# Kernel optimization log

Hardware: AMD Instinct MI355X
Metric: run time of the kernel (lower is better)

## Reference

```python
import jax, jax.numpy as jnp
import numpy as np

T, B, S, H, E, V = 100, 64, 602, 1024, 512, 10000


def setup_inputs() -> dict:
    key = jax.random.key(0)
    ks = jax.random.split(key, 12)
    s = 0.02  # small init scale for numerical stability through tanh/sigmoid
    return {
        "tgt": jax.random.randint(ks[0], (T, B, 1), 0, V),
        "memory_bank": jax.random.normal(ks[1], (S, B, H), jnp.float32),
        "h0": jax.random.normal(ks[2], (2, B, H), jnp.float32) * 0.1,
        "c0": jax.random.normal(ks[3], (2, B, H), jnp.float32) * 0.1,
        "embedding": jax.random.normal(ks[4], (V, E), jnp.float32) * s,
        "Wi0": jax.random.normal(ks[5], (4 * H, E + H), jnp.float32) * s,
        "Wh0": jax.random.normal(ks[6], (4 * H, H), jnp.float32) * s,
        "bi0": jnp.zeros((4 * H,), jnp.float32),
        "bh0": jnp.zeros((4 * H,), jnp.float32),
        "Wi1": jax.random.normal(ks[7], (4 * H, H), jnp.float32) * s,
        "Wh1": jax.random.normal(ks[8], (4 * H, H), jnp.float32) * s,
        "bi1": jnp.zeros((4 * H,), jnp.float32),
        "bh1": jnp.zeros((4 * H,), jnp.float32),
        "W_attn": jax.random.normal(ks[9], (H, H), jnp.float32) * s,
        "W_out": jax.random.normal(ks[10], (H, 2 * H), jnp.float32) * s,
    }


def _lstm_cell(x, h, c, Wi, Wh, bi, bh):
    # PyTorch LSTM gate order: i, f, g, o
    g = x @ Wi.T + h @ Wh.T + bi + bh
    i, f, gg, o = jnp.split(g, 4, axis=-1)
    c2 = jax.nn.sigmoid(f) * c + jax.nn.sigmoid(i) * jnp.tanh(gg)
    h2 = jax.nn.sigmoid(o) * jnp.tanh(c2)
    return h2, c2


def reference(tgt, memory_bank, h0, c0, embedding, Wi0, Wh0, bi0, bh0,
              Wi1, Wh1, bi1, bh1, W_attn, W_out):
    emb = embedding[tgt[:, :, 0]]            # [T, B, E]
    M = jnp.transpose(memory_bank, (1, 0, 2))  # [B, S, H]

    def step(carry, e_t):
        hl0, hl1, cl0, cl1, feed = carry
        x = jnp.concatenate([e_t, feed], axis=-1)        # input feeding
        nh0, nc0 = _lstm_cell(x, hl0, cl0, Wi0, Wh0, bi0, bh0)
        nh1, nc1 = _lstm_cell(nh0, hl1, cl1, Wi1, Wh1, bi1, bh1)
        # GlobalAttention 'general': score = (h W) . m
        q = nh1 @ W_attn.T                                # [B, H]
        align = jnp.einsum('bh,bsh->bs', q, M)            # [B, S]
        a = jax.nn.softmax(align, axis=-1)
        ctx = jnp.einsum('bs,bsh->bh', a, M)              # [B, H]
        out = jnp.tanh(jnp.concatenate([ctx, nh1], -1) @ W_out.T)  # attn_h
        return (nh0, nh1, nc0, nc1, out), (out, a)

    init = (h0[0], h0[1], c0[0], c0[1], jnp.zeros((B, H), emb.dtype))
    (_, _, _, _, _), (outs, attns) = jax.lax.scan(step, init, emb)
    return outs, attns  # [T,B,H], [T,B,S]
```

## Files before the change

kernel.cpp:

```cpp
#include <hip/hip_runtime.h>


#define DI __device__ __forceinline__

typedef __attribute__((ext_vector_type(4))) short s4v;
typedef __attribute__((ext_vector_type(8))) short s8v;
typedef __attribute__((ext_vector_type(4))) float f4v;

DI float b2f(short u) {
  unsigned int x = ((unsigned int)(unsigned short)u) << 16;
  float f; __builtin_memcpy(&f, &x, 4); return f;
}
DI short f2b(float f) {
  unsigned int x; __builtin_memcpy(&x, &f, 4);
  return (short)((x + 0x7fffu + ((x >> 16) & 1u)) >> 16);
}
DI s8v cat8(s4v lo, s4v hi) {
  s8v r; r[0]=lo[0];r[1]=lo[1];r[2]=lo[2];r[3]=lo[3];
  r[4]=hi[0];r[5]=hi[1];r[6]=hi[2];r[7]=hi[3]; return r;
}
DI f4v mfma16(s8v a, s8v b, f4v c) {
  return __builtin_amdgcn_mfma_f32_16x16x32_bf16(a, b, c, 0, 0, 0);
}
DI float sigm(float x) { return 1.f / (1.f + __expf(-x)); }

DI unsigned long long ld64c(const void* p) {
  return __hip_atomic_load((const unsigned long long*)p, __ATOMIC_RELAXED,
                           __HIP_MEMORY_SCOPE_SYSTEM);
}
DI void st64c(void* p, unsigned long long v) {
  __hip_atomic_store((unsigned long long*)p, v, __ATOMIC_RELAXED,
                     __HIP_MEMORY_SCOPE_SYSTEM);
}
DI float ldfc(const float* p) {
  return __hip_atomic_load(p, __ATOMIC_RELAXED, __HIP_MEMORY_SCOPE_SYSTEM);
}
DI void stfc(float* p, float v) {
  __hip_atomic_store(p, v, __ATOMIC_RELAXED, __HIP_MEMORY_SCOPE_SYSTEM);
}
DI void st16c(short* p, short v) {
  asm volatile("global_store_short %0, %1, off sc0 sc1"
               :: "v"(p), "v"((unsigned int)(unsigned short)v) : "memory");
}
union U64S { unsigned long long u; short s[4]; };
union U64F { unsigned long long u; float f[2]; };


__global__ void cvt_bf16(const float* __restrict__ src, short* __restrict__ dst, long n8) {
  long i = (long)blockIdx.x * blockDim.x + threadIdx.x;
  long stride = (long)gridDim.x * blockDim.x;
  for (; i < n8; i += stride) {
    const float* s = src + i * 8;
    s8v o;
    #pragma unroll
    for (int j = 0; j < 8; ++j) o[j] = f2b(s[j]);
    *(s8v*)(dst + i * 8) = o;
  }
}

__global__ void pack_w(const float* __restrict__ WA, int Ka,
                       const float* __restrict__ WB, int Kb,
                       short* __restrict__ dst, int N, long total) {
  long i = (long)blockIdx.x * blockDim.x + threadIdx.x;
  long stride = (long)gridDim.x * blockDim.x;
  for (; i < total; i += stride) {
    int c = (int)(i & 3);
    long r = i >> 2;
    int n = (int)(r % N);
    int kt = (int)(r / N);
    int k = kt * 32 + c * 8;
    const float* s = (k < Ka) ? (WA + (size_t)n * Ka + k)
                              : (WB + (size_t)n * Kb + (k - Ka));
    s8v o;
    #pragma unroll
    for (int j = 0; j < 8; ++j) o[j] = f2b(s[j]);
    *(s8v*)(dst + r * 32 + c * 8) = o;
  }
}

__global__ __launch_bounds__(64) void emb_gather(const int* __restrict__ tgt,
                                                 const float* __restrict__ emb,
                                                 short* __restrict__ dst) {
  int tb = blockIdx.x;
  int idx = tgt[tb];
  const float* s = emb + (size_t)idx * 512 + threadIdx.x * 8;
  s8v o;
  #pragma unroll
  for (int j = 0; j < 8; ++j) o[j] = f2b(s[j]);
  *(s8v*)(dst + (size_t)tb * 512 + threadIdx.x * 8) = o;
}

__global__ void init_state(const float* __restrict__ h0, const float* __restrict__ c0,
                           short* __restrict__ h0r, short* __restrict__ h1r,
                           float* __restrict__ c0buf, float* __restrict__ c1buf,
                           short* __restrict__ feedr) {
  int i = blockIdx.x * 256 + threadIdx.x;
  if (i < 65536) {
    h0r[i] = f2b(h0[i]);
    h1r[i] = f2b(h0[65536 + i]);
    c0buf[i] = c0[i];
    c1buf[i] = c0[65536 + i];
    feedr[i] = 0;
  }
}


template <int NG>
DI void kloop(const short* __restrict__ A, int ld, int nkt,
              const short* __restrict__ Wp, size_t wkt,
              f4v* acc, int rA, int g) {
  if (nkt <= 0) return;
  const short* ap = A + (size_t)rA * ld + 4 * g;
  s4v alo = *(const s4v*)ap, ahi = *(const s4v*)(ap + 16);
  s4v blo[NG], bhi[NG];
  #pragma unroll
  for (int t = 0; t < NG; ++t) {
    blo[t] = *(const s4v*)(Wp + (size_t)t * 32768);
    bhi[t] = *(const s4v*)(Wp + (size_t)t * 32768 + 16);
  }
  for (int kt = 0; kt < nkt - 1; ++kt) {
    const short* apn = ap + (kt + 1) * 32;
    const short* bpn = Wp + (size_t)(kt + 1) * wkt;
    s4v nalo = *(const s4v*)apn, nahi = *(const s4v*)(apn + 16);
    s4v nblo[NG], nbhi[NG];
    #pragma unroll
    for (int t = 0; t < NG; ++t) {
      nblo[t] = *(const s4v*)(bpn + (size_t)t * 32768);
      nbhi[t] = *(const s4v*)(bpn + (size_t)t * 32768 + 16);
    }
    s8v a = cat8(alo, ahi);
    #pragma unroll
    for (int t = 0; t < NG; ++t) acc[t] = mfma16(a, cat8(blo[t], bhi[t]), acc[t]);
    alo = nalo; ahi = nahi;
    #pragma unroll
    for (int t = 0; t < NG; ++t) { blo[t] = nblo[t]; bhi[t] = nbhi[t]; }
  }
  s8v a = cat8(alo, ahi);
  #pragma unroll
  for (int t = 0; t < NG; ++t) acc[t] = mfma16(a, cat8(blo[t], bhi[t]), acc[t]);
}

template <int NG>
DI void seg_gemm(const short* __restrict__ A0, int ld0, int n0,
                 const short* __restrict__ A1, int ld1, int n1,
                 const short* __restrict__ A2, int ld2, int n2,
                 const short* __restrict__ wbase, size_t wkt,
                 int k0, int k1, f4v* acc, int rA, int g) {
  int s = 0;
  {
    int a = k0 > s ? k0 : s, b = k1 < (s + n0) ? k1 : (s + n0);
    if (a < b) kloop<NG>(A0 + (size_t)(a - s) * 32, ld0, b - a,
                         wbase + (size_t)a * wkt, wkt, acc, rA, g);
    s += n0;
  }
  {
    int a = k0 > s ? k0 : s, b = k1 < (s + n1) ? k1 : (s + n1);
    if (a < b) kloop<NG>(A1 + (size_t)(a - s) * 32, ld1, b - a,
                         wbase + (size_t)a * wkt, wkt, acc, rA, g);
    s += n1;
  }
  if (n2 > 0) {
    int a = k0 > s ? k0 : s, b = k1 < (s + n2) ? k1 : (s + n2);
    if (a < b) kloop<NG>(A2 + (size_t)(a - s) * 32, ld2, b - a,
                         wbase + (size_t)a * wkt, wkt, acc, rA, g);
  }
}

template <int NG>
DI void wave_reduce(f4v* acc, float* smem, int w, int l) {
  #pragma unroll
  for (int t4 = 0; t4 < NG; ++t4)
    *(f4v*)&smem[(w * 64 + l) * 20 + t4 * 4] = acc[t4];
  __syncthreads();
  if (w == 0) {
    #pragma unroll
    for (int t4 = 0; t4 < NG; ++t4) {
      f4v s0 = *(f4v*)&smem[l * 20 + t4 * 4];
      #pragma unroll
      for (int ww = 1; ww < 4; ++ww) {
        f4v v = *(f4v*)&smem[(ww * 64 + l) * 20 + t4 * 4];
        #pragma unroll
        for (int j = 0; j < 4; ++j) s0[j] += v[j];
      }
      acc[t4] = s0;
    }
  }
}


DI void gbar(int* bar, int bid, int want) {
  __syncthreads();
  if (threadIdx.x == 0) {
    int* leaf = bar + (bid >> 4) * 64;
    if (__hip_atomic_fetch_add(leaf, 1, __ATOMIC_RELAXED,
                               __HIP_MEMORY_SCOPE_AGENT) == want * 16 - 1) {
      if (__hip_atomic_fetch_add(bar + 1024, 1, __ATOMIC_RELAXED,
                                 __HIP_MEMORY_SCOPE_AGENT) == want * 16 - 1) {
        __hip_atomic_store(bar + 1088, want, __ATOMIC_RELAXED,
                           __HIP_MEMORY_SCOPE_AGENT);
      }
    }
    while (__hip_atomic_load(bar + 1088, __ATOMIC_RELAXED,
                             __HIP_MEMORY_SCOPE_AGENT) < want)
      __builtin_amdgcn_s_sleep(2);
  }
  __syncthreads();
}


__global__ __launch_bounds__(256, 1) void decoder_k(
    const short* __restrict__ W0p, const short* __restrict__ W1p,
    const short* __restrict__ Wop, const short* __restrict__ Wap,
    const short* __restrict__ emba,
    const float* __restrict__ bi0, const float* __restrict__ bh0,
    const float* __restrict__ bi1, const float* __restrict__ bh1,
    short* h0r, short* h1r, short* feedr, short* ctxr, short* qb,
    float* c0b, float* c1b, float* alg, float* part,
    const short* __restrict__ Mb, const float* __restrict__ memf,
    float* out, int useMb, int* bar) {
  __shared__ float smem[5248];
  const int bid = blockIdx.x, tid = threadIdx.x;
  const int w = tid >> 6, l = tid & 63, r15 = l & 15, g = l >> 4;
  const int cs = bid & 63, rt = bid >> 6;
  int barno = 0;
  f4v z = {0.f, 0.f, 0.f, 0.f};

  for (int t = 0; t < 100; ++t) {
    const size_t scur = (size_t)t * 65536, snxt = (size_t)(t + 1) * 65536;

    {
      f4v acc[4] = {z, z, z, z};
      const short* wbase = W0p + (size_t)(cs * 16 + r15) * 32 + 4 * g;
      seg_gemm<4>(emba + (size_t)t * 64 * 512, 512, 16,
                  feedr + scur, 1024, 32, h0r + scur, 1024, 32,
                  wbase, (size_t)4096 * 32, w * 20, w * 20 + 20,
                  acc, rt * 16 + r15, g);
      wave_reduce<4>(acc, smem, w, l);
      if (w == 0) {
        int h = cs * 16 + r15;
        float bs0 = bi0[h] + bh0[h];
        float bs1 = bi0[1024 + h] + bh0[1024 + h];
        float bs2 = bi0[2048 + h] + bh0[2048 + h];
        float bs3 = bi0[3072 + h] + bh0[3072 + h];
        #pragma unroll
        for (int q = 0; q < 4; ++q) {
          int brow = rt * 16 + g * 4 + q;
          size_t off = (size_t)brow * 1024 + h;
          float iv = acc[0][q] + bs0, fv = acc[1][q] + bs1;
          float gv = acc[2][q] + bs2, ov = acc[3][q] + bs3;
          float cn = sigm(fv) * c0b[off] + sigm(iv) * tanhf(gv);
          float hn = sigm(ov) * tanhf(cn);
          c0b[off] = cn;
          st16c(h0r + snxt + off, f2b(hn));
        }
      }
      gbar(bar, bid, ++barno);
    }

    {
      f4v acc[4] = {z, z, z, z};
      const short* wbase = W1p + (size_t)(cs * 16 + r15) * 32 + 4 * g;
      seg_gemm<4>(h0r + snxt, 1024, 32, h1r + scur, 1024, 32,
                  (const short*)nullptr, 0, 0,
                  wbase, (size_t)4096 * 32, w * 16, w * 16 + 16,
                  acc, rt * 16 + r15, g);
      wave_reduce<4>(acc, smem, w, l);
      if (w == 0) {
        int h = cs * 16 + r15;
        float bs0 = bi1[h] + bh1[h];
        float bs1 = bi1[1024 + h] + bh1[1024 + h];
        float bs2 = bi1[2048 + h] + bh1[2048 + h];
        float bs3 = bi1[3072 + h] + bh1[3072 + h];
        #pragma unroll
        for (int q = 0; q < 4; ++q) {
          int brow = rt * 16 + g * 4 + q;
          size_t off = (size_t)brow * 1024 + h;
          float iv = acc[0][q] + bs0, fv = acc[1][q] + bs1;
          float gv = acc[2][q] + bs2, ov = acc[3][q] + bs3;
          float cn = sigm(fv) * c1b[off] + sigm(iv) * tanhf(gv);
          float hn = sigm(ov) * tanhf(cn);
          c1b[off] = cn;
          st16c(h1r + snxt + off, f2b(hn));
        }
      }
      gbar(bar, bid, ++barno);
    }

    {
      f4v acc[1] = {z};
      const short* wbase = Wap + (size_t)(cs * 16 + r15) * 32 + 4 * g;
      seg_gemm<1>(h1r + snxt, 1024, 32, (const short*)nullptr, 0, 0,
                  (const short*)nullptr, 0, 0,
                  wbase, (size_t)1024 * 32, w * 8, w * 8 + 8,
                  acc, rt * 16 + r15, g);
      wave_reduce<1>(acc, smem, w, l);
      if (w == 0) {
        int nb = cs * 16 + r15;
        #pragma unroll
        for (int q = 0; q < 4; ++q) {
          int brow = rt * 16 + g * 4 + q;
          st16c(qb + (size_t)brow * 1024 + nb, f2b(acc[0][q]));
        }
      }
      gbar(bar, bid, ++barno);
    }

    {
      int b = bid & 63, chunk = bid >> 6;
      int s0 = chunk * 151;
      int send = 602 < s0 + 151 ? 602 : s0 + 151;
      const short* qp = qb + (size_t)b * 1024 + l * 16;
      float qf[16];
      #pragma unroll
      for (int c4 = 0; c4 < 4; ++c4) {
        U64S x; x.u = ld64c(qp + c4 * 4);
        #pragma unroll
        for (int j = 0; j < 4; ++j) qf[c4 * 4 + j] = b2f(x.s[j]);
      }
      float o[16];
      #pragma unroll
      for (int j = 0; j < 16; ++j) o[j] = 0.f;
      for (int s = s0 + w; s < send; s += 8) {
        int s2 = s + 4;
        bool has2 = s2 < send;
        float mv0[16], mv1[16];
        if (useMb) {
          const short* mp0 = Mb + ((size_t)s * 64 + b) * 1024 + l * 16;
          s8v a0 = *(const s8v*)mp0, a1 = *(const s8v*)(mp0 + 8);
          const short* mp1 = Mb + ((size_t)(has2 ? s2 : s) * 64 + b) * 1024 + l * 16;
          s8v b0 = *(const s8v*)mp1, b1 = *(const s8v*)(mp1 + 8);
          #pragma unroll
          for (int j = 0; j < 8; ++j) {
            mv0[j] = b2f(a0[j]); mv0[8 + j] = b2f(a1[j]);
            mv1[j] = b2f(b0[j]); mv1[8 + j] = b2f(b1[j]);
          }
        } else {
          const float* mp0 = memf + ((size_t)s * 64 + b) * 1024 + l * 16;
          const float* mp1 = memf + ((size_t)(has2 ? s2 : s) * 64 + b) * 1024 + l * 16;
          f4v a0 = *(const f4v*)mp0, a1 = *(const f4v*)(mp0 + 4);
          f4v a2 = *(const f4v*)(mp0 + 8), a3 = *(const f4v*)(mp0 + 12);
          f4v b0 = *(const f4v*)mp1, b1 = *(const f4v*)(mp1 + 4);
          f4v b2 = *(const f4v*)(mp1 + 8), b3 = *(const f4v*)(mp1 + 12);
          #pragma unroll
          for (int j = 0; j < 4; ++j) {
            mv0[j] = a0[j]; mv0[4 + j] = a1[j]; mv0[8 + j] = a2[j]; mv0[12 + j] = a3[j];
            mv1[j] = b0[j]; mv1[4 + j] = b1[j]; mv1[8 + j] = b2[j]; mv1[12 + j] = b3[j];
          }
        }
        float d0 = 0.f, d1 = 0.f;
        #pragma unroll
        for (int j = 0; j < 16; ++j) { d0 += qf[j] * mv0[j]; d1 += qf[j] * mv1[j]; }
        #pragma unroll
        for (int off = 32; off; off >>= 1) {
          d0 += __shfl_down(d0, off);
          d1 += __shfl_down(d1, off);
        }
        d0 = __shfl(d0, 0); d1 = __shfl(d1, 0);
        if (l == 0) {
          stfc(alg + b * 602 + s, d0);
          if (has2) stfc(alg + b * 602 + s2, d1);
        }
        float p0 = __expf(fminf(d0, 80.f) - 8.f);
        float p1 = has2 ? __expf(fminf(d1, 80.f) - 8.f) : 0.f;
        #pragma unroll
        for (int j = 0; j < 16; ++j) o[j] += p0 * mv0[j] + p1 * mv1[j];
      }
      float* pp = part + (size_t)(b * 16 + chunk * 4 + w) * 1024;
      #pragma unroll
      for (int j4 = 0; j4 < 8; ++j4) {
        U64F x; x.f[0] = o[j4 * 2]; x.f[1] = o[j4 * 2 + 1];
        st64c(pp + l * 16 + j4 * 2, x.u);
      }
      __syncthreads();
      if (tid == 0) {
        int* acnt = bar + 2048 + b * 16;
        __hip_atomic_fetch_add(acnt, 1, __ATOMIC_RELAXED,
                               __HIP_MEMORY_SCOPE_AGENT);
        while (__hip_atomic_load(acnt, __ATOMIC_RELAXED,
                                 __HIP_MEMORY_SCOPE_AGENT) < 4 * (t + 1))
          __builtin_amdgcn_s_sleep(1);
      }
      __syncthreads();
      {
        float* pv = smem;
        float* red = smem + 604;
        const float* al = alg + b * 602;
        float lm = -1e30f;
        for (int i = tid; i < 602; i += 256) {
          float v = ldfc(al + i); pv[i] = v; lm = fmaxf(lm, v);
        }
        #pragma unroll
        for (int o2 = 32; o2; o2 >>= 1) lm = fmaxf(lm, __shfl_down(lm, o2));
        if (l == 0) red[w] = lm;
        __syncthreads();
        float M = fmaxf(fmaxf(red[0], red[1]), fmaxf(red[2], red[3]));
        float ls = 0.f;
        for (int i = tid; i < 602; i += 256) {
          float e = __expf(pv[i] - M); pv[i] = e; ls += e;
        }
        #pragma unroll
        for (int o2 = 32; o2; o2 >>= 1) ls += __shfl_down(ls, o2);
        __syncthreads();
        if (l == 0) red[4 + w] = ls;
        __syncthreads();
        float L = red[4] + red[5] + red[6] + red[7];
        float scale = __expf(8.f - M) / L;
        if (tid < 128) {
          int h = chunk * 256 + tid * 2;
          float a0 = 0.f, a1 = 0.f;
          #pragma unroll
          for (int p = 0; p < 16; ++p) {
            U64F x; x.u = ld64c(part + (size_t)(b * 16 + p) * 1024 + h);
            a0 += x.f[0]; a1 += x.f[1];
          }
          short* cp = ctxr + snxt + (size_t)b * 1024 + h;
          st16c(cp, f2b(a0 * scale));
          st16c(cp + 1, f2b(a1 * scale));
        }
        float invL = 1.f / L;
        float* attns = out + 6553600 + (size_t)t * 64 * 602;
        for (int i = s0 + tid; i < send; i += 256)
          attns[b * 602 + i] = pv[i] * invL;
      }
      gbar(bar, bid, ++barno);
    }

    {
      f4v acc[1] = {z};
      const short* wbase = Wop + (size_t)(cs * 16 + r15) * 32 + 4 * g;
      seg_gemm<1>(ctxr + snxt, 1024, 32, h1r + snxt, 1024, 32,
                  (const short*)nullptr, 0, 0,
                  wbase, (size_t)1024 * 32, w * 16, w * 16 + 16,
                  acc, rt * 16 + r15, g);
      wave_reduce<1>(acc, smem, w, l);
      if (w == 0) {
        int nb = cs * 16 + r15;
        float* outp = out + (size_t)t * 65536;
        #pragma unroll
        for (int q = 0; q < 4; ++q) {
          int brow = rt * 16 + g * 4 + q;
          size_t off = (size_t)brow * 1024 + nb;
          float v = tanhf(acc[0][q]);
          outp[off] = v;
          st16c(feedr + snxt + off, f2b(v));
        }
      }
      gbar(bar, bid, ++barno);
    }
  }
}


extern "C" void kernel_launch(void* const* d_in, const int* in_sizes, int n_in,
                              void* d_out, int out_size, void* d_ws, size_t ws_size,
                              hipStream_t stream) {
  const int*   tgt  = (const int*)  d_in[0];
  const float* mem  = (const float*)d_in[1];
  const float* h0   = (const float*)d_in[2];
  const float* c0   = (const float*)d_in[3];
  const float* embw = (const float*)d_in[4];
  const float* Wi0  = (const float*)d_in[5];
  const float* Wh0  = (const float*)d_in[6];
  const float* bi0  = (const float*)d_in[7];
  const float* bh0  = (const float*)d_in[8];
  const float* Wi1  = (const float*)d_in[9];
  const float* Wh1  = (const float*)d_in[10];
  const float* bi1  = (const float*)d_in[11];
  const float* bh1  = (const float*)d_in[12];
  const float* Wat  = (const float*)d_in[13];
  const float* Wou  = (const float*)d_in[14];
  float* out = (float*)d_out;

  char* base = (char*)d_ws;
  size_t off = 0;
  auto alloc = [&](size_t bytes) -> void* {
    void* p = base + off;
    off += (bytes + 255) & ~(size_t)255;
    return p;
  };
  const size_t RING = (size_t)101 * 65536;
  int* bar = (int*)alloc(16384);
  short* qb   = (short*)alloc(65536 * 2);
  float* c0b  = (float*)alloc(65536 * 4);
  float* c1b  = (float*)alloc(65536 * 4);
  float* alg  = (float*)alloc((size_t)64 * 602 * 4);
  float* part = (float*)alloc((size_t)64 * 16 * 1024 * 4);
  short* emba = (short*)alloc((size_t)100 * 64 * 512 * 2);
  short* Wap  = (short*)alloc((size_t)32 * 1024 * 32 * 2);
  short* Wop  = (short*)alloc((size_t)64 * 1024 * 32 * 2);
  short* W1p  = (short*)alloc((size_t)64 * 4096 * 32 * 2);
  short* W0p  = (short*)alloc((size_t)80 * 4096 * 32 * 2);
  short* h0r  = (short*)alloc(RING * 2);
  short* h1r  = (short*)alloc(RING * 2);
  short* feedr= (short*)alloc(RING * 2);
  short* ctxr = (short*)alloc(RING * 2);
  const size_t MBE = (size_t)602 * 64 * 1024;
  bool useMb = (off + MBE * 2 + 256) <= ws_size;
  short* Mb = useMb ? (short*)alloc(MBE * 2) : nullptr;

  hipMemsetAsync(bar, 0, 16384, stream);
  hipLaunchKernelGGL(emb_gather, dim3(6400), dim3(64), 0, stream, tgt, embw, emba);
  hipLaunchKernelGGL(pack_w, dim3(2048), dim3(256), 0, stream, Wi0, 1536, Wh0, 1024,
                     W0p, 4096, (long)80 * 4096 * 4);
  hipLaunchKernelGGL(pack_w, dim3(2048), dim3(256), 0, stream, Wi1, 1024, Wh1, 1024,
                     W1p, 4096, (long)64 * 4096 * 4);
  hipLaunchKernelGGL(pack_w, dim3(1024), dim3(256), 0, stream, Wou, 2048, Wou, 2048,
                     Wop, 1024, (long)64 * 1024 * 4);
  hipLaunchKernelGGL(pack_w, dim3(512), dim3(256), 0, stream, Wat, 1024, Wat, 1024,
                     Wap, 1024, (long)32 * 1024 * 4);
  hipLaunchKernelGGL(init_state, dim3(256), dim3(256), 0, stream, h0, c0,
                     h0r, h1r, c0b, c1b, feedr);
  if (useMb)
    hipLaunchKernelGGL(cvt_bf16, dim3(2048), dim3(256), 0, stream, mem, Mb,
                       (long)(MBE / 8));

  hipLaunchKernelGGL(decoder_k, dim3(256), dim3(256), 0, stream,
                     W0p, W1p, Wop, Wap, emba,
                     bi0, bh0, bi1, bh1,
                     h0r, h1r, feedr, ctxr, qb,
                     c0b, c1b, alg, part,
                     Mb, mem, out, (int)useMb,
                     bar);
}
```

Before: 7.787 ms.

## Replace tree grid barrier with flag-based master barrier and fixed-shift softmax sums

The grid barrier's atomic counter tree is replaced by per-block flag stores, which block 0 polls with all its threads before publishing a release flag. The attention softmax no longer re-reads all scores to find a max and sum. Each chunk now stores exp(score-8) values plus a partial sum, and the final normalisation divides by the total of the four chunk sums. This removes a serial per-batch reduction and lowers barrier contention, but relies on the fixed shift of 8 and the clamp at 80 being numerically safe instead of using a true max.

Result: no change. 7.833 ms (+0.6%).

```diff
diff --git a/kernel.cpp b/kernel.cpp
--- a/kernel.cpp
+++ b/kernel.cpp
@@ -36,6 +36,12 @@
   return __hip_atomic_load(p, __ATOMIC_RELAXED, __HIP_MEMORY_SCOPE_SYSTEM);
 }
 DI void stfc(float* p, float v) {
+  __hip_atomic_store(p, v, __ATOMIC_RELAXED, __HIP_MEMORY_SCOPE_SYSTEM);
+}
+DI int ld32c(const int* p) {
+  return __hip_atomic_load(p, __ATOMIC_RELAXED, __HIP_MEMORY_SCOPE_SYSTEM);
+}
+DI void st32c(int* p, int v) {
   __hip_atomic_store(p, v, __ATOMIC_RELAXED, __HIP_MEMORY_SCOPE_SYSTEM);
 }
 DI void st16c(short* p, short v) {
@@ -190,19 +196,20 @@
 
 DI void gbar(int* bar, int bid, int want) {
   __syncthreads();
-  if (threadIdx.x == 0) {
-    int* leaf = bar + (bid >> 4) * 64;
-    if (__hip_atomic_fetch_add(leaf, 1, __ATOMIC_RELAXED,
-                               __HIP_MEMORY_SCOPE_AGENT) == want * 16 - 1) {
-      if (__hip_atomic_fetch_add(bar + 1024, 1, __ATOMIC_RELAXED,
-                                 __HIP_MEMORY_SCOPE_AGENT) == want * 16 - 1) {
-        __hip_atomic_store(bar + 1088, want, __ATOMIC_RELAXED,
-                           __HIP_MEMORY_SCOPE_AGENT);
-      }
-    }
-    while (__hip_atomic_load(bar + 1088, __ATOMIC_RELAXED,
-                             __HIP_MEMORY_SCOPE_AGENT) < want)
-      __builtin_amdgcn_s_sleep(2);
+  int tid = threadIdx.x;
+  if (bid == 0) {
+    for (;;) {
+      int ok = 1;
+      if (tid > 0) ok = (ld32c(bar + tid * 16) >= want);
+      if (__syncthreads_and(ok)) break;
+      __builtin_amdgcn_s_sleep(1);
+    }
+    if (tid == 0) st32c(bar + 4096, want);
+  } else {
+    if (tid == 0) {
+      st32c(bar + bid * 16, want);
+      while (ld32c(bar + 4096) < want) __builtin_amdgcn_s_sleep(2);
+    }
   }
   __syncthreads();
 }
@@ -215,7 +222,7 @@
     const float* __restrict__ bi0, const float* __restrict__ bh0,
     const float* __restrict__ bi1, const float* __restrict__ bh1,
     short* h0r, short* h1r, short* feedr, short* ctxr, short* qb,
-    float* c0b, float* c1b, float* alg, float* part,
+    float* c0b, float* c1b, float* alg, float* part, float* csum,
     const short* __restrict__ Mb, const float* __restrict__ memf,
     float* out, int useMb, int* bar) {
   __shared__ float smem[5248];
@@ -320,6 +327,7 @@
       float o[16];
       #pragma unroll
       for (int j = 0; j < 16; ++j) o[j] = 0.f;
+      float ls8 = 0.f;
       for (int s = s0 + w; s < send; s += 8) {
         int s2 = s + 4;
         bool has2 = s2 < send;
@@ -356,12 +364,13 @@
           d1 += __shfl_down(d1, off);
         }
         d0 = __shfl(d0, 0); d1 = __shfl(d1, 0);
-        if (l == 0) {
-          stfc(alg + b * 602 + s, d0);
-          if (has2) stfc(alg + b * 602 + s2, d1);
-        }
         float p0 = __expf(fminf(d0, 80.f) - 8.f);
         float p1 = has2 ? __expf(fminf(d1, 80.f) - 8.f) : 0.f;
+        if (l == 0) {
+          stfc(alg + b * 602 + s, p0);
+          if (has2) stfc(alg + b * 602 + s2, p1);
+        }
+        ls8 += p0 + p1;
         #pragma unroll
         for (int j = 0; j < 16; ++j) o[j] += p0 * mv0[j] + p1 * mv1[j];
       }
@@ -371,9 +380,14 @@
         U64F x; x.f[0] = o[j4 * 2]; x.f[1] = o[j4 * 2 + 1];
         st64c(pp + l * 16 + j4 * 2, x.u);
       }
+      if (l == 0) smem[5120 + w] = ls8;
+      __syncthreads();
+      if (tid == 0)
+        stfc(csum + b * 4 + chunk,
+             smem[5120] + smem[5121] + smem[5122] + smem[5123]);
       __syncthreads();
       if (tid == 0) {
-        int* acnt = bar + 2048 + b * 16;
+        int* acnt = bar + 4352 + b * 16;
         __hip_atomic_fetch_add(acnt, 1, __ATOMIC_RELAXED,
                                __HIP_MEMORY_SCOPE_AGENT);
         while (__hip_atomic_load(acnt, __ATOMIC_RELAXED,
@@ -382,29 +396,9 @@
       }
       __syncthreads();
       {
-        float* pv = smem;
-        float* red = smem + 604;
-        const float* al = alg + b * 602;
-        float lm = -1e30f;
-        for (int i = tid; i < 602; i += 256) {
-          float v = ldfc(al + i); pv[i] = v; lm = fmaxf(lm, v);
-        }
-        #pragma unroll
-        for (int o2 = 32; o2; o2 >>= 1) lm = fmaxf(lm, __shfl_down(lm, o2));
-        if (l == 0) red[w] = lm;
-        __syncthreads();
-        float M = fmaxf(fmaxf(red[0], red[1]), fmaxf(red[2], red[3]));
-        float ls = 0.f;
-        for (int i = tid; i < 602; i += 256) {
-          float e = __expf(pv[i] - M); pv[i] = e; ls += e;
-        }
-        #pragma unroll
-        for (int o2 = 32; o2; o2 >>= 1) ls += __shfl_down(ls, o2);
-        __syncthreads();
-        if (l == 0) red[4 + w] = ls;
-        __syncthreads();
-        float L = red[4] + red[5] + red[6] + red[7];
-        float scale = __expf(8.f - M) / L;
+        const float* cs4 = csum + b * 4;
+        float L8 = ldfc(cs4) + ldfc(cs4 + 1) + ldfc(cs4 + 2) + ldfc(cs4 + 3);
+        float invL = 1.f / L8;
         if (tid < 128) {
           int h = chunk * 256 + tid * 2;
           float a0 = 0.f, a1 = 0.f;
@@ -414,13 +408,12 @@
             a0 += x.f[0]; a1 += x.f[1];
           }
           short* cp = ctxr + snxt + (size_t)b * 1024 + h;
-          st16c(cp, f2b(a0 * scale));
-          st16c(cp + 1, f2b(a1 * scale));
-        }
-        float invL = 1.f / L;
+          st16c(cp, f2b(a0 * invL));
+          st16c(cp + 1, f2b(a1 * invL));
+        }
         float* attns = out + 6553600 + (size_t)t * 64 * 602;
         for (int i = s0 + tid; i < send; i += 256)
-          attns[b * 602 + i] = pv[i] * invL;
+          attns[b * 602 + i] = ldfc(alg + b * 602 + i) * invL;
       }
       gbar(bar, bid, ++barno);
     }
@@ -479,8 +472,9 @@
     return p;
   };
   const size_t RING = (size_t)101 * 65536;
-  int* bar = (int*)alloc(16384);
+  int* bar = (int*)alloc(32768);
   short* qb   = (short*)alloc(65536 * 2);
+  float* csum = (float*)alloc(64 * 4 * 4);
   float* c0b  = (float*)alloc(65536 * 4);
   float* c1b  = (float*)alloc(65536 * 4);
   float* alg  = (float*)alloc((size_t)64 * 602 * 4);
@@ -498,7 +492,7 @@
   bool useMb = (off + MBE * 2 + 256) <= ws_size;
   short* Mb = useMb ? (short*)alloc(MBE * 2) : nullptr;
 
-  hipMemsetAsync(bar, 0, 16384, stream);
+  hipMemsetAsync(bar, 0, 32768, stream);
   hipLaunchKernelGGL(emb_gather, dim3(6400), dim3(64), 0, stream, tgt, embw, emba);
   hipLaunchKernelGGL(pack_w, dim3(2048), dim3(256), 0, stream, Wi0, 1536, Wh0, 1024,
                      W0p, 4096, (long)80 * 4096 * 4);
@@ -518,7 +512,7 @@
                      W0p, W1p, Wop, Wap, emba,
                      bi0, bh0, bi1, bh1,
                      h0r, h1r, feedr, ctxr, qb,
-                     c0b, c1b, alg, part,
+                     c0b, c1b, alg, part, csum,
                      Mb, mem, out, (int)useMb,
                      bar);
 }
```
